# Kernel tuning notes

Hardware: AMD Instinct MI355X
Metric: run time of the kernel (lower is better)

Reference implementation:

```python
import jax, jax.numpy as jnp
import numpy as np

TEMP = 0.5

def setup_inputs() -> dict:
    key = jax.random.key(0)
    k1, k2 = jax.random.split(key)
    B, D = 4096, 256
    x_i = jax.random.normal(k1, (B, D), dtype=jnp.float32)
    x_j = jax.random.normal(k2, (B, D), dtype=jnp.float32)
    return {"x_i": x_i, "x_j": x_j}

def reference(x_i, x_j):
    B = x_i.shape[0]
    z = jnp.concatenate([x_i, x_j], axis=0)  # [2B, D]
    # cosine similarity = normalized dot product (eps matches torch default 1e-8)
    zn = z / jnp.maximum(jnp.linalg.norm(z, axis=-1, keepdims=True), 1e-8)
    sim = zn @ zn.T  # [2B, 2B]
    sim_ij = jnp.diagonal(sim, offset=B)
    sim_ji = jnp.diagonal(sim, offset=-B)
    pos = jnp.concatenate([sim_ij, sim_ji], axis=0)  # [2B]
    # neg_mask = ~eye: zero out self-similarity in the denominator
    exp_sim = jnp.exp(sim / TEMP)
    idx = jnp.arange(2 * B)
    denom = jnp.sum(exp_sim, axis=1) - exp_sim[idx, idx]  # masked row-sum
    loss = jnp.sum(-(pos / TEMP - jnp.log(denom))) / (2 * B)
    return loss
```

## Files before the change

kernel.cpp:

```cpp
#include <hip/hip_runtime.h>
#include <stdint.h>

#define B_ROWS 4096
#define D 256
#define NTOT (2 * B_ROWS)
#define TEMP_INV 2.0f

#define NSPLIT 16
#define BM 128
#define COLS_PER_BLOCK (NTOT / NSPLIT)
#define JT_COUNT (COLS_PER_BLOCK / 64)

typedef __attribute__((ext_vector_type(8))) short bf16x8;
typedef __attribute__((ext_vector_type(4))) float f32x4;
typedef __attribute__((ext_vector_type(4))) unsigned short us4;

typedef const __attribute__((address_space(1))) char gch;
typedef __attribute__((address_space(3))) char lch;

static __device__ __forceinline__ unsigned short f2bf(float f) {
  union { float f; unsigned u; } v; v.f = f;
  unsigned r = v.u + 0x7FFFu + ((v.u >> 16) & 1u);
  return (unsigned short)(r >> 16);
}
static __device__ __forceinline__ float bf2f(unsigned short u) {
  union { unsigned u; float f; } v; v.u = ((unsigned)u) << 16;
  return v.f;
}

__global__ __launch_bounds__(256) void k_prep(const float* __restrict__ xi,
                                              const float* __restrict__ xj,
                                              unsigned short* __restrict__ zn) {
  int row = blockIdx.x * 4 + (threadIdx.x >> 6);
  int lane = threadIdx.x & 63;
  const float* src = (row < B_ROWS) ? (xi + (size_t)row * D)
                                    : (xj + (size_t)(row - B_ROWS) * D);
  float4 v = ((const float4*)src)[lane];
  float ss = v.x * v.x + v.y * v.y + v.z * v.z + v.w * v.w;
  #pragma unroll
  for (int m = 1; m < 64; m <<= 1) ss += __shfl_xor(ss, m, 64);
  float inv = 1.0f / fmaxf(sqrtf(ss), 1e-8f);
  us4 o;
  o.x = f2bf(v.x * inv); o.y = f2bf(v.y * inv);
  o.z = f2bf(v.z * inv); o.w = f2bf(v.w * inv);
  *(us4*)(zn + (size_t)row * D + lane * 4) = o;
}

__global__ __launch_bounds__(256) void k_pos(const unsigned short* __restrict__ zn,
                                             float* __restrict__ pos) {
  int i = blockIdx.x * 4 + (threadIdx.x >> 6);
  int lane = threadIdx.x & 63;
  int j = (i < B_ROWS) ? (i + B_ROWS) : (i - B_ROWS);
  us4 a = *(const us4*)(zn + (size_t)i * D + lane * 4);
  us4 b = *(const us4*)(zn + (size_t)j * D + lane * 4);
  float d = bf2f(a.x) * bf2f(b.x) + bf2f(a.y) * bf2f(b.y) +
            bf2f(a.z) * bf2f(b.z) + bf2f(a.w) * bf2f(b.w);
  #pragma unroll
  for (int m = 1; m < 64; m <<= 1) d += __shfl_xor(d, m, 64);
  if (lane == 0) pos[i] = d;
}

__global__ __launch_bounds__(256) void k_gemm(const unsigned short* __restrict__ zn,
                                              float* __restrict__ rowsum) {
  __shared__ char lds[64 * 512];
  int rb = (int)(blockIdx.x / NSPLIT) * BM;
  int cb = (int)(blockIdx.x % NSPLIT) * COLS_PER_BLOCK;
  int w = threadIdx.x >> 6;
  int lane = threadIdx.x & 63;
  int hi = lane >> 4, lo = lane & 15;

  const char* znb = (const char*)zn;

  bf16x8 a0[8], a1[8];
  int r0 = rb + w * 32 + lo;
  #pragma unroll
  for (int f = 0; f < 8; f++) {
    a0[f] = *(const bf16x8*)(znb + (size_t)r0 * 512 + f * 64 + hi * 16);
    a1[f] = *(const bf16x8*)(znb + (size_t)(r0 + 16) * 512 + f * 64 + hi * 16);
  }

  float rs[2][4] = {{0.f, 0.f, 0.f, 0.f}, {0.f, 0.f, 0.f, 0.f}};

  for (int jt = 0; jt < JT_COUNT; jt++) {
    int colbase = cb + jt * 64;
    __syncthreads();
    #pragma unroll
    for (int it = 0; it < 8; it++) {
      int local = w * 8192 + it * 1024 + lane * 16;
      int src = local ^ (((local >> 9) & 7) << 4);
      __builtin_amdgcn_global_load_lds(
          (gch*)(znb + (size_t)colbase * 512 + src),
          (lch*)(lds + w * 8192 + it * 1024), 16, 0, 0);
    }
    asm volatile("s_waitcnt vmcnt(0)");
    __syncthreads();

    #pragma unroll
    for (int nt = 0; nt < 4; nt++) {
      int ldrow = nt * 16 + lo;
      int sw = (ldrow & 7) << 4;
      bf16x8 b[8];
      #pragma unroll
      for (int f = 0; f < 8; f++) {
        int off = ldrow * 512 + f * 64 + hi * 16;
        b[f] = *(const bf16x8*)(lds + (off ^ sw));
      }
      f32x4 acc0 = {0.f, 0.f, 0.f, 0.f}, acc1 = {0.f, 0.f, 0.f, 0.f};
      #pragma unroll
      for (int f = 0; f < 8; f++) {
        acc0 = __builtin_amdgcn_mfma_f32_16x16x32_bf16(a0[f], b[f], acc0, 0, 0, 0);
        acc1 = __builtin_amdgcn_mfma_f32_16x16x32_bf16(a1[f], b[f], acc1, 0, 0, 0);
      }
      #pragma unroll
      for (int r = 0; r < 4; r++) {
        rs[0][r] += __expf(TEMP_INV * acc0[r]);
        rs[1][r] += __expf(TEMP_INV * acc1[r]);
      }
    }
  }

  #pragma unroll
  for (int m = 1; m < 16; m <<= 1) {
    #pragma unroll
    for (int t = 0; t < 2; t++)
      #pragma unroll
      for (int r = 0; r < 4; r++)
        rs[t][r] += __shfl_xor(rs[t][r], m, 64);
  }
  if (lo == 0) {
    #pragma unroll
    for (int t = 0; t < 2; t++)
      #pragma unroll
      for (int r = 0; r < 4; r++)
        atomicAdd(&rowsum[rb + w * 32 + t * 16 + hi * 4 + r], rs[t][r]);
  }
}

__global__ __launch_bounds__(256) void k_final(const float* __restrict__ rowsum,
                                               const float* __restrict__ pos,
                                               float* __restrict__ out) {
  int i = blockIdx.x * 256 + threadIdx.x;
  float denom = rowsum[i] - 7.3890560989306495f;
  float t = __logf(denom) - TEMP_INV * pos[i];
  #pragma unroll
  for (int m = 1; m < 64; m <<= 1) t += __shfl_xor(t, m, 64);
  __shared__ float wsum[4];
  int w = threadIdx.x >> 6, lane = threadIdx.x & 63;
  if (lane == 0) wsum[w] = t;
  __syncthreads();
  if (threadIdx.x == 0) {
    float s = wsum[0] + wsum[1] + wsum[2] + wsum[3];
    atomicAdd(out, s * (1.0f / NTOT));
  }
}

extern "C" void kernel_launch(void* const* d_in, const int* in_sizes, int n_in,
                              void* d_out, int out_size, void* d_ws, size_t ws_size,
                              hipStream_t stream) {
  const float* xi = (const float*)d_in[0];
  const float* xj = (const float*)d_in[1];

  unsigned short* zn = (unsigned short*)d_ws;
  char* base = (char*)d_ws + (size_t)NTOT * D * 2;
  float* rowsum = (float*)base;
  float* pos = (float*)(base + (size_t)NTOT * 4);

  hipMemsetAsync(rowsum, 0, NTOT * sizeof(float), stream);
  hipMemsetAsync(d_out, 0, out_size * sizeof(float), stream);

  k_prep<<<NTOT / 4, 256, 0, stream>>>(xi, xj, zn);
  k_pos<<<NTOT / 4, 256, 0, stream>>>(zn, pos);
  k_gemm<<<(NTOT / BM) * NSPLIT, 256, 0, stream>>>(zn, rowsum);
  k_final<<<NTOT / 256, 256, 0, stream>>>(rowsum, pos, (float*)d_out);
}
```

Measured before the change: 107.9 us.

## Fuse prep and pos kernels, double-buffer GEMM tiles, drop atomics and memsets

```diff
diff --git a/kernel.cpp b/kernel.cpp
--- a/kernel.cpp
+++ b/kernel.cpp
@@ -4,12 +4,11 @@
 #define B_ROWS 4096
 #define D 256
 #define NTOT (2 * B_ROWS)
-#define TEMP_INV 2.0f
-
 #define NSPLIT 16
-#define BM 128
+#define BM 256
 #define COLS_PER_BLOCK (NTOT / NSPLIT)
 #define JT_COUNT (COLS_PER_BLOCK / 64)
+#define C_SCALE 2.8853900817779268f
 
 typedef __attribute__((ext_vector_type(8))) short bf16x8;
 typedef __attribute__((ext_vector_type(4))) float f32x4;
@@ -23,100 +22,122 @@
   unsigned r = v.u + 0x7FFFu + ((v.u >> 16) & 1u);
   return (unsigned short)(r >> 16);
 }
-static __device__ __forceinline__ float bf2f(unsigned short u) {
-  union { unsigned u; float f; } v; v.u = ((unsigned)u) << 16;
-  return v.f;
-}
 
 __global__ __launch_bounds__(256) void k_prep(const float* __restrict__ xi,
                                               const float* __restrict__ xj,
-                                              unsigned short* __restrict__ zn) {
-  int row = blockIdx.x * 4 + (threadIdx.x >> 6);
+                                              unsigned short* __restrict__ zn,
+                                              unsigned short* __restrict__ zns,
+                                              float* __restrict__ pos,
+                                              float* __restrict__ out) {
+  if (blockIdx.x == 0 && threadIdx.x == 0) out[0] = 0.0f;
+  int p = blockIdx.x * 4 + (threadIdx.x >> 6);
   int lane = threadIdx.x & 63;
-  const float* src = (row < B_ROWS) ? (xi + (size_t)row * D)
-                                    : (xj + (size_t)(row - B_ROWS) * D);
-  float4 v = ((const float4*)src)[lane];
-  float ss = v.x * v.x + v.y * v.y + v.z * v.z + v.w * v.w;
+  float4 a = ((const float4*)(xi + (size_t)p * D))[lane];
+  float4 b = ((const float4*)(xj + (size_t)p * D))[lane];
+  float sa = a.x * a.x + a.y * a.y + a.z * a.z + a.w * a.w;
+  float sb = b.x * b.x + b.y * b.y + b.z * b.z + b.w * b.w;
+  float ab = a.x * b.x + a.y * b.y + a.z * b.z + a.w * b.w;
   #pragma unroll
-  for (int m = 1; m < 64; m <<= 1) ss += __shfl_xor(ss, m, 64);
-  float inv = 1.0f / fmaxf(sqrtf(ss), 1e-8f);
-  us4 o;
-  o.x = f2bf(v.x * inv); o.y = f2bf(v.y * inv);
-  o.z = f2bf(v.z * inv); o.w = f2bf(v.w * inv);
-  *(us4*)(zn + (size_t)row * D + lane * 4) = o;
+  for (int m = 1; m < 64; m <<= 1) {
+    sa += __shfl_xor(sa, m, 64);
+    sb += __shfl_xor(sb, m, 64);
+    ab += __shfl_xor(ab, m, 64);
+  }
+  float ia = 1.0f / fmaxf(sqrtf(sa), 1e-8f);
+  float ib = 1.0f / fmaxf(sqrtf(sb), 1e-8f);
+  float na[4] = {a.x * ia, a.y * ia, a.z * ia, a.w * ia};
+  float nb[4] = {b.x * ib, b.y * ib, b.z * ib, b.w * ib};
+  us4 oa, ob, sa4, sb4;
+  oa.x = f2bf(na[0]); oa.y = f2bf(na[1]); oa.z = f2bf(na[2]); oa.w = f2bf(na[3]);
+  ob.x = f2bf(nb[0]); ob.y = f2bf(nb[1]); ob.z = f2bf(nb[2]); ob.w = f2bf(nb[3]);
+  sa4.x = f2bf(na[0] * C_SCALE); sa4.y = f2bf(na[1] * C_SCALE);
+  sa4.z = f2bf(na[2] * C_SCALE); sa4.w = f2bf(na[3] * C_SCALE);
+  sb4.x = f2bf(nb[0] * C_SCALE); sb4.y = f2bf(nb[1] * C_SCALE);
+  sb4.z = f2bf(nb[2] * C_SCALE); sb4.w = f2bf(nb[3] * C_SCALE);
+  *(us4*)(zn  + (size_t)p * D + lane * 4) = oa;
+  *(us4*)(zn  + (size_t)(p + B_ROWS) * D + lane * 4) = ob;
+  *(us4*)(zns + (size_t)p * D + lane * 4) = sa4;
+  *(us4*)(zns + (size_t)(p + B_ROWS) * D + lane * 4) = sb4;
+  if (lane == 0) {
+    float d = ab * ia * ib;
+    pos[p] = d;
+    pos[p + B_ROWS] = d;
+  }
 }
 
-__global__ __launch_bounds__(256) void k_pos(const unsigned short* __restrict__ zn,
-                                             float* __restrict__ pos) {
-  int i = blockIdx.x * 4 + (threadIdx.x >> 6);
-  int lane = threadIdx.x & 63;
-  int j = (i < B_ROWS) ? (i + B_ROWS) : (i - B_ROWS);
-  us4 a = *(const us4*)(zn + (size_t)i * D + lane * 4);
-  us4 b = *(const us4*)(zn + (size_t)j * D + lane * 4);
-  float d = bf2f(a.x) * bf2f(b.x) + bf2f(a.y) * bf2f(b.y) +
-            bf2f(a.z) * bf2f(b.z) + bf2f(a.w) * bf2f(b.w);
-  #pragma unroll
-  for (int m = 1; m < 64; m <<= 1) d += __shfl_xor(d, m, 64);
-  if (lane == 0) pos[i] = d;
-}
-
-__global__ __launch_bounds__(256) void k_gemm(const unsigned short* __restrict__ zn,
-                                              float* __restrict__ rowsum) {
-  __shared__ char lds[64 * 512];
+__global__ __launch_bounds__(512, 4) void k_gemm(const unsigned short* __restrict__ zn,
+                                                 const unsigned short* __restrict__ zns,
+                                                 float* __restrict__ part) {
+  __shared__ char lds[2 * 32768];
   int rb = (int)(blockIdx.x / NSPLIT) * BM;
-  int cb = (int)(blockIdx.x % NSPLIT) * COLS_PER_BLOCK;
+  int cs = (int)(blockIdx.x % NSPLIT);
+  int cb = cs * COLS_PER_BLOCK;
   int w = threadIdx.x >> 6;
   int lane = threadIdx.x & 63;
   int hi = lane >> 4, lo = lane & 15;
 
-  const char* znb = (const char*)zn;
+  const char* znb  = (const char*)zn;
+  const char* znsb = (const char*)zns;
 
   bf16x8 a0[8], a1[8];
   int r0 = rb + w * 32 + lo;
   #pragma unroll
   for (int f = 0; f < 8; f++) {
-    a0[f] = *(const bf16x8*)(znb + (size_t)r0 * 512 + f * 64 + hi * 16);
-    a1[f] = *(const bf16x8*)(znb + (size_t)(r0 + 16) * 512 + f * 64 + hi * 16);
+    a0[f] = *(const bf16x8*)(znsb + (size_t)r0 * 512 + f * 64 + hi * 16);
+    a1[f] = *(const bf16x8*)(znsb + (size_t)(r0 + 16) * 512 + f * 64 + hi * 16);
   }
+
+  int rdbase[8];
+  #pragma unroll
+  for (int f = 0; f < 8; f++)
+    rdbase[f] = lo * 512 + ((f * 64 + hi * 16) ^ ((lo & 7) << 4));
 
   float rs[2][4] = {{0.f, 0.f, 0.f, 0.f}, {0.f, 0.f, 0.f, 0.f}};
 
-  for (int jt = 0; jt < JT_COUNT; jt++) {
-    int colbase = cb + jt * 64;
-    __syncthreads();
+  auto stage = [&](int bufofs, int colrow) {
     #pragma unroll
-    for (int it = 0; it < 8; it++) {
-      int local = w * 8192 + it * 1024 + lane * 16;
+    for (int c = 0; c < 4; c++) {
+      int local = w * 4096 + c * 1024 + lane * 16;
       int src = local ^ (((local >> 9) & 7) << 4);
       __builtin_amdgcn_global_load_lds(
-          (gch*)(znb + (size_t)colbase * 512 + src),
-          (lch*)(lds + w * 8192 + it * 1024), 16, 0, 0);
+          (gch*)(znb + (size_t)colrow * 512 + src),
+          (lch*)(lds + bufofs + w * 4096 + c * 1024), 16, 0, 0);
     }
-    asm volatile("s_waitcnt vmcnt(0)");
-    __syncthreads();
-
+  };
+  auto compute = [&](int bufofs) {
     #pragma unroll
     for (int nt = 0; nt < 4; nt++) {
-      int ldrow = nt * 16 + lo;
-      int sw = (ldrow & 7) << 4;
-      bf16x8 b[8];
-      #pragma unroll
-      for (int f = 0; f < 8; f++) {
-        int off = ldrow * 512 + f * 64 + hi * 16;
-        b[f] = *(const bf16x8*)(lds + (off ^ sw));
-      }
       f32x4 acc0 = {0.f, 0.f, 0.f, 0.f}, acc1 = {0.f, 0.f, 0.f, 0.f};
       #pragma unroll
       for (int f = 0; f < 8; f++) {
-        acc0 = __builtin_amdgcn_mfma_f32_16x16x32_bf16(a0[f], b[f], acc0, 0, 0, 0);
-        acc1 = __builtin_amdgcn_mfma_f32_16x16x32_bf16(a1[f], b[f], acc1, 0, 0, 0);
+        bf16x8 b = *(const bf16x8*)(lds + rdbase[f] + bufofs + nt * 8192);
+        acc0 = __builtin_amdgcn_mfma_f32_16x16x32_bf16(a0[f], b, acc0, 0, 0, 0);
+        acc1 = __builtin_amdgcn_mfma_f32_16x16x32_bf16(a1[f], b, acc1, 0, 0, 0);
       }
       #pragma unroll
       for (int r = 0; r < 4; r++) {
-        rs[0][r] += __expf(TEMP_INV * acc0[r]);
-        rs[1][r] += __expf(TEMP_INV * acc1[r]);
+        float e0, e1;
+        asm("v_exp_f32 %0, %1" : "=v"(e0) : "v"(acc0[r]));
+        asm("v_exp_f32 %0, %1" : "=v"(e1) : "v"(acc1[r]));
+        rs[0][r] += e0;
+        rs[1][r] += e1;
       }
     }
+  };
+  auto drain_barrier = []() {
+    asm volatile("s_waitcnt vmcnt(0)" ::: "memory");
+    __syncthreads();
+  };
+
+  stage(0, cb);
+  drain_barrier();
+  for (int jt = 0; jt < JT_COUNT; jt += 2) {
+    if (jt + 1 < JT_COUNT) stage(32768, cb + (jt + 1) * 64);
+    compute(0);
+    drain_barrier();
+    if (jt + 2 < JT_COUNT) stage(0, cb + (jt + 2) * 64);
+    compute(32768);
+    drain_barrier();
   }
 
   #pragma unroll
@@ -132,26 +153,27 @@
     for (int t = 0; t < 2; t++)
       #pragma unroll
       for (int r = 0; r < 4; r++)
-        atomicAdd(&rowsum[rb + w * 32 + t * 16 + hi * 4 + r], rs[t][r]);
+        part[(size_t)cs * NTOT + rb + w * 32 + t * 16 + hi * 4 + r] = rs[t][r];
   }
 }
 
-__global__ __launch_bounds__(256) void k_final(const float* __restrict__ rowsum,
+__global__ __launch_bounds__(256) void k_final(const float* __restrict__ part,
                                                const float* __restrict__ pos,
                                                float* __restrict__ out) {
   int i = blockIdx.x * 256 + threadIdx.x;
-  float denom = rowsum[i] - 7.3890560989306495f;
-  float t = __logf(denom) - TEMP_INV * pos[i];
+  float s = 0.f;
+  #pragma unroll
+  for (int c = 0; c < NSPLIT; c++) s += part[(size_t)c * NTOT + i];
+  float denom = s - 7.3890560989306495f;
+  float t = __logf(denom) - 2.0f * pos[i];
   #pragma unroll
   for (int m = 1; m < 64; m <<= 1) t += __shfl_xor(t, m, 64);
   __shared__ float wsum[4];
   int w = threadIdx.x >> 6, lane = threadIdx.x & 63;
   if (lane == 0) wsum[w] = t;
   __syncthreads();
-  if (threadIdx.x == 0) {
-    float s = wsum[0] + wsum[1] + wsum[2] + wsum[3];
-    atomicAdd(out, s * (1.0f / NTOT));
-  }
+  if (threadIdx.x == 0)
+    atomicAdd(out, (wsum[0] + wsum[1] + wsum[2] + wsum[3]) * (1.0f / NTOT));
 }
 
 extern "C" void kernel_launch(void* const* d_in, const int* in_sizes, int n_in,
@@ -160,16 +182,13 @@
   const float* xi = (const float*)d_in[0];
   const float* xj = (const float*)d_in[1];
 
-  unsigned short* zn = (unsigned short*)d_ws;
-  char* base = (char*)d_ws + (size_t)NTOT * D * 2;
-  float* rowsum = (float*)base;
-  float* pos = (float*)(base + (size_t)NTOT * 4);
+  unsigned short* zn  = (unsigned short*)d_ws;
+  unsigned short* zns = zn + (size_t)NTOT * D;
+  char* base = (char*)(zns + (size_t)NTOT * D);
+  float* part = (float*)base;
+  float* pos  = (float*)(base + (size_t)NSPLIT * NTOT * 4);
 
-  hipMemsetAsync(rowsum, 0, NTOT * sizeof(float), stream);
-  hipMemsetAsync(d_out, 0, out_size * sizeof(float), stream);
-
-  k_prep<<<NTOT / 4, 256, 0, stream>>>(xi, xj, zn);
-  k_pos<<<NTOT / 4, 256, 0, stream>>>(zn, pos);
-  k_gemm<<<(NTOT / BM) * NSPLIT, 256, 0, stream>>>(zn, rowsum);
-  k_final<<<NTOT / 256, 256, 0, stream>>>(rowsum, pos, (float*)d_out);
+  k_prep<<<B_ROWS / 4, 256, 0, stream>>>(xi, xj, zn, zns, pos, (float*)d_out);
+  k_gemm<<<(NTOT / BM) * NSPLIT, 512, 0, stream>>>(zn, zns, part);
+  k_final<<<NTOT / 256, 256, 0, stream>>>(part, pos, (float*)d_out);
 }
```

After: 100.3 us. 7.0% less time.
